# Kernel tuning notes

Hardware: AMD Instinct MI355X
Metric: run time of the kernel (lower is better)

## Reference

```python
import jax, jax.numpy as jnp
import numpy as np

N = 50000      # nodes
E = 800000     # edges (avg degree 16)
D = 128        # hidden_dim (= in_dim)
H = 8          # heads
DH = D // H    # head dim = 16
L = 2          # num_layers=1 -> ModuleList has 2 layers (extra append)
LN_EPS = 1e-5


def layer_norm(x, w, b):
    m = jnp.mean(x, axis=-1, keepdims=True)
    v = jnp.mean((x - m) ** 2, axis=-1, keepdims=True)
    return (x - m) * jax.lax.rsqrt(v + LN_EPS) * w + b


def setup_inputs() -> dict:
    key = jax.random.key(0)
    ks = jax.random.split(key, 16)
    s = 0.05

    def nrm(k, shape):
        return jax.random.normal(k, shape, jnp.float32) * s

    inp = {
        "h": jax.random.normal(ks[0], (N, D), jnp.float32),
        "src": jax.random.randint(ks[1], (E,), 0, N),
        "dst": jax.random.randint(ks[2], (E,), 0, N),
        "W_emb": nrm(ks[3], (D, D)),
        "Wq": nrm(ks[4], (L, D, D)), "bq": jnp.zeros((L, D), jnp.float32),
        "Wk": nrm(ks[5], (L, D, D)), "bk": jnp.zeros((L, D), jnp.float32),
        "Wv": nrm(ks[6], (L, D, D)), "bv": jnp.zeros((L, D), jnp.float32),
        "Wo": nrm(ks[7], (L, D, D)), "bo": jnp.zeros((L, D), jnp.float32),
        "ln1_w": jnp.ones((L, D), jnp.float32), "ln1_b": jnp.zeros((L, D), jnp.float32),
        "Wf1": nrm(ks[8], (L, D, 2 * D)), "bf1": jnp.zeros((L, 2 * D), jnp.float32),
        "Wf2": nrm(ks[9], (L, 2 * D, D)), "bf2": jnp.zeros((L, D), jnp.float32),
        "ln2_w": jnp.ones((L, D), jnp.float32), "ln2_b": jnp.zeros((L, D), jnp.float32),
    }
    return inp


def reference(h, src, dst, W_emb, Wq, bq, Wk, bk, Wv, bv, Wo, bo,
              ln1_w, ln1_b, Wf1, bf1, Wf2, bf2, ln2_w, ln2_b):
    n = h.shape[0]
    scale = 1.0 / np.sqrt(DH)  # np.sqrt(self.out_dim), out_dim = head dim = 16
    h = h @ W_emb  # embedding_h (no bias)
    for l in range(L):
        q = (h @ Wq[l] + bq[l]).reshape(n, H, DH)
        k = (h @ Wk[l] + bk[l]).reshape(n, H, DH)
        v = (h @ Wv[l] + bv[l]).reshape(n, H, DH)
        # per-edge score: K[src] . Q[dst], scaled, clamped, exponentiated
        s = jnp.einsum('ehd,ehd->eh', k[src], q[dst]) * scale  # [E,H]
        s = jnp.exp(jnp.clip(s, -5.0, 5.0))
        # scatter-sum weighted V and normalizer z into dst nodes
        wV = jax.ops.segment_sum(v[src] * s[:, :, None], dst, num_segments=n)  # [N,H,DH]
        z = jax.ops.segment_sum(s, dst, num_segments=n)                        # [N,H]
        attn = (wV / (z[:, :, None] + 1e-6)).reshape(n, D)
        hx = layer_norm(h + attn @ Wo[l] + bo[l], ln1_w[l], ln1_b[l])
        ffn = jax.nn.relu(hx @ Wf1[l] + bf1[l]) @ Wf2[l] + bf2[l]  # dropout inactive (eval)
        h = layer_norm(hx + ffn, ln2_w[l], ln2_b[l])
    return h
```

## Files before the change

kernel.cpp:

```cpp
#include <hip/hip_runtime.h>
#include <math.h>

static constexpr int N_NODES = 50000;
static constexpr int N_EDGES = 800000;
static constexpr int DMODEL  = 128;
static constexpr int MTILES  = N_NODES / 16;
static constexpr int CAPLOG  = 6;
static constexpr int ESPLIT  = 400384;

typedef __attribute__((ext_vector_type(8))) short short8;
typedef __attribute__((ext_vector_type(4))) float float4v;

__device__ __forceinline__ unsigned short f2bf(float f) {
    unsigned u = __builtin_bit_cast(unsigned, f);
    u += 0x7fffu + ((u >> 16) & 1u);
    return (unsigned short)(u >> 16);
}
__device__ __forceinline__ float bf2f(unsigned short b) {
    unsigned u = ((unsigned)b) << 16;
    return __builtin_bit_cast(float, u);
}

struct PrepSeg { const float* src; int K; int N; int dstOff; };
struct PrepArgs { PrepSeg seg[13]; };

__global__ void prep_kernel(PrepArgs pa, unsigned short* wf, int* counts)
{
    if (blockIdx.y == 13) {
        for (int i = blockIdx.x * 256 + threadIdx.x; i < N_NODES; i += 128 * 256)
            counts[i] = 0;
        return;
    }
    PrepSeg sg = pa.seg[blockIdx.y];
    int e = blockIdx.x * 256 + threadIdx.x;
    int total = sg.K * sg.N;
    if (e >= total) return;
    int n = e % sg.N;
    int k = e / sg.N;
    int ks = sg.K >> 5;
    int nt = n >> 4, c = n & 15, s = k >> 5, q = (k >> 3) & 3, jj = k & 7;
    int di = sg.dstOff + (nt * ks + s) * 512 + q * 128 + c * 8 + jj;
    wf[di] = f2bf(sg.src[e]);
}

__device__ __forceinline__ void scatter_body(
    const int* __restrict__ src, const int* __restrict__ dst,
    int* counts, int* eslot, int ebeg, int eend)
{
    int blk = ebeg + blockIdx.x * 1024;
    if (blk >= eend) return;
    int base = blk + threadIdx.x;
    int d[4], s[4];
    bool v[4];
#pragma unroll
    for (int k = 0; k < 4; ++k) {
        int e = base + k * 256;
        v[k] = e < eend;
        int ec = v[k] ? e : ebeg;
        d[k] = dst[ec];
        s[k] = src[ec];
    }
#pragma unroll
    for (int k = 0; k < 4; ++k) {
        if (v[k]) {
            int r = atomicAdd(&counts[d[k]], 1);
            eslot[(d[k] << CAPLOG) + r] = s[k];
        }
    }
}

template<int KSTEPS, int NT, int EPI, bool AF32, bool WRF, bool WRB>
__device__ __forceinline__ void gemm_body(
    const void* __restrict__ Ap, const unsigned short* __restrict__ Wfc,
    const float* __restrict__ bias, const float* res,
    float* Cf, unsigned short* Cb,
    const float* __restrict__ lnw, const float* __restrict__ lnb,
    int ldA, int ldC, int mtiles, int colBase)
{
    const int lane = threadIdx.x & 63;
    const int c = lane & 15;
    const int q = lane >> 4;

    __shared__ unsigned short smB[NT * KSTEPS * 512];
    {
        const int totalVec = NT * KSTEPS * 64;
        const uint4* gsrc = (const uint4*)Wfc;
        uint4* sdst = (uint4*)smB;
#pragma unroll
        for (int i = threadIdx.x; i < totalVec; i += 256)
            sdst[i] = gsrc[i];
    }
    __syncthreads();

    short8 bfrag[NT][KSTEPS];
#pragma unroll
    for (int nt = 0; nt < NT; ++nt)
#pragma unroll
        for (int s = 0; s < KSTEPS; ++s)
            bfrag[nt][s] = *(const short8*)(smB + (nt * KSTEPS + s) * 512 + lane * 8);

    float bb[NT];
#pragma unroll
    for (int nt = 0; nt < NT; ++nt)
        bb[nt] = bias ? bias[colBase + nt * 16 + c] : 0.f;

    float lw[NT], lb[NT];
    if (EPI == 3) {
#pragma unroll
        for (int nt = 0; nt < NT; ++nt) {
            lw[nt] = lnw[nt * 16 + c];
            lb[nt] = lnb[nt * 16 + c];
        }
    }

    const int wid = blockIdx.x * 4 + (threadIdx.x >> 6);
    const int nw  = gridDim.x * 4;

    for (int mt = wid; mt < mtiles; mt += nw) {
        const int row0 = mt * 16;
        short8 afrag[KSTEPS];
        if (AF32) {
            const float* A32 = (const float*)Ap;
#pragma unroll
            for (int s = 0; s < KSTEPS; ++s) {
                const float4* p = (const float4*)(A32 + (size_t)(row0 + c) * ldA + s * 32 + q * 8);
                float4 x0 = p[0], x1 = p[1];
                short8 a;
                a[0] = (short)f2bf(x0.x); a[1] = (short)f2bf(x0.y);
                a[2] = (short)f2bf(x0.z); a[3] = (short)f2bf(x0.w);
                a[4] = (short)f2bf(x1.x); a[5] = (short)f2bf(x1.y);
                a[6] = (short)f2bf(x1.z); a[7] = (short)f2bf(x1.w);
                afrag[s] = a;
            }
        } else {
            const unsigned short* Ab = (const unsigned short*)Ap;
#pragma unroll
            for (int s = 0; s < KSTEPS; ++s)
                afrag[s] = *(const short8*)(Ab + (size_t)(row0 + c) * ldA + s * 32 + q * 8);
        }

        float4v acc[NT];
#pragma unroll
        for (int nt = 0; nt < NT; ++nt) acc[nt] = (float4v)0.f;
#pragma unroll
        for (int s = 0; s < KSTEPS; ++s)
#pragma unroll
            for (int nt = 0; nt < NT; ++nt)
                acc[nt] = __builtin_amdgcn_mfma_f32_16x16x32_bf16(afrag[s], bfrag[nt][s], acc[nt], 0, 0, 0);

#pragma unroll
        for (int nt = 0; nt < NT; ++nt) {
            const int col = colBase + nt * 16 + c;
#pragma unroll
            for (int r = 0; r < 4; ++r) {
                const int grow = row0 + q * 4 + r;
                float v = acc[nt][r] + bb[nt];
                if (EPI == 2 || EPI == 3) v += res[(size_t)grow * ldC + col];
                if (EPI == 1) v = fmaxf(v, 0.f);
                acc[nt][r] = v;
            }
        }

        if (EPI == 3) {
#pragma unroll
            for (int r = 0; r < 4; ++r) {
                float s = 0.f, ss = 0.f;
#pragma unroll
                for (int nt = 0; nt < NT; ++nt) {
                    float v = acc[nt][r];
                    s += v; ss = fmaf(v, v, ss);
                }
#pragma unroll
                for (int o = 1; o < 16; o <<= 1) {
                    s  += __shfl_xor(s, o, 64);
                    ss += __shfl_xor(ss, o, 64);
                }
                float m   = s * (1.0f / 128.0f);
                float var = ss * (1.0f / 128.0f) - m * m;
                float rs  = rsqrtf(var + 1e-5f);
                const int grow = row0 + q * 4 + r;
#pragma unroll
                for (int nt = 0; nt < NT; ++nt) {
                    float v = (acc[nt][r] - m) * rs * lw[nt] + lb[nt];
                    if (WRF) Cf[(size_t)grow * ldC + nt * 16 + c] = v;
                    if (WRB) Cb[(size_t)grow * ldC + nt * 16 + c] = f2bf(v);
                }
            }
        } else {
#pragma unroll
            for (int nt = 0; nt < NT; ++nt) {
                const int col = colBase + nt * 16 + c;
#pragma unroll
                for (int r = 0; r < 4; ++r) {
                    const int grow = row0 + q * 4 + r;
                    if (WRF) Cf[(size_t)grow * ldC + col] = acc[nt][r];
                    if (WRB) Cb[(size_t)grow * ldC + col] = f2bf(acc[nt][r]);
                }
            }
        }
    }
}

__global__ __launch_bounds__(256, 2)
void emb_sc_gemm(const float* __restrict__ A, const unsigned short* __restrict__ Wf,
                 float* Cf, unsigned short* Cb, int mtiles,
                 const int* __restrict__ src, const int* __restrict__ dst,
                 int* counts, int* eslot, int ebeg, int eend)
{
    if (blockIdx.y == 1) {
        scatter_body(src, dst, counts, eslot, ebeg, eend);
        return;
    }
    gemm_body<4, 8, 0, true, true, true>(
        A, Wf, nullptr, nullptr, Cf, Cb, nullptr, nullptr, 128, 128, mtiles, 0);
}

struct QkvPtrs { const float* bias[3]; unsigned short* out[3]; int ldc[3]; };

__global__ __launch_bounds__(256, 2)
void qkv_sc_gemm(const unsigned short* __restrict__ A, const unsigned short* __restrict__ WfBase,
                 QkvPtrs ptrs, int mtiles,
                 const int* __restrict__ src, const int* __restrict__ dst,
                 int* counts, int* eslot, int ebeg, int eend)
{
    if (blockIdx.y == 3) {
        scatter_body(src, dst, counts, eslot, ebeg, eend);
        return;
    }
    const int sel = blockIdx.y;
    gemm_body<4, 8, 0, false, false, true>(
        A, WfBase + (size_t)sel * 32768, ptrs.bias[sel], nullptr,
        nullptr, ptrs.out[sel], nullptr, nullptr, 128, ptrs.ldc[sel], mtiles, 0);
}

template<bool WRB>
__global__ __launch_bounds__(256, 2)
void blk_kernel(const unsigned short* __restrict__ attn,
                const unsigned short* __restrict__ W0,
                const unsigned short* __restrict__ W1,
                const unsigned short* __restrict__ W2,
                const float* __restrict__ b0,
                const float* __restrict__ b1, const float* __restrict__ b2,
                const float* __restrict__ l1wv, const float* __restrict__ l1bv,
                const float* __restrict__ l2wv, const float* __restrict__ l2bv,
                const float* __restrict__ res,
                float* Cf, unsigned short* Cb,
                int mtiles)
{
    const int lane = threadIdx.x & 63;
    const int c = lane & 15;
    const int q = lane >> 4;
    const int w = threadIdx.x >> 6;

    __shared__ unsigned short hxf[4 * 64 * 8];
    __shared__ unsigned short exf[8 * 64 * 8];
    __shared__ float sred1[16][4][2];
    __shared__ float sred2[16][4][2];

    short8 b0f[2][4];
#pragma unroll
    for (int nt = 0; nt < 2; ++nt)
#pragma unroll
        for (int s = 0; s < 4; ++s)
            b0f[nt][s] = *(const short8*)(W0 + (size_t)((w * 2 + nt) * 4 + s) * 512 + lane * 8);

    short8 b1f[4][4];
#pragma unroll
    for (int nt = 0; nt < 4; ++nt)
#pragma unroll
        for (int s = 0; s < 4; ++s)
            b1f[nt][s] = *(const short8*)(W1 + (size_t)((w * 4 + nt) * 4 + s) * 512 + lane * 8);

    short8 b2f[2][8];
#pragma unroll
    for (int nt = 0; nt < 2; ++nt)
#pragma unroll
        for (int s = 0; s < 8; ++s)
            b2f[nt][s] = *(const short8*)(W2 + (size_t)((w * 2 + nt) * 8 + s) * 512 + lane * 8);

    float bb0[2], l1w[2], l1b[2], bb2[2], l2w[2], l2b[2];
#pragma unroll
    for (int nt = 0; nt < 2; ++nt) {
        int col = w * 32 + nt * 16 + c;
        bb0[nt] = b0[col];  l1w[nt] = l1wv[col]; l1b[nt] = l1bv[col];
        bb2[nt] = b2[col];  l2w[nt] = l2wv[col]; l2b[nt] = l2bv[col];
    }
    float bb1[4];
#pragma unroll
    for (int nt = 0; nt < 4; ++nt) bb1[nt] = b1[w * 64 + nt * 16 + c];

    const int iters = (mtiles + gridDim.x - 1) / gridDim.x;
    for (int it = 0; it < iters; ++it) {
        const int mt = blockIdx.x + it * gridDim.x;
        const bool active = mt < mtiles;
        const int row0 = (active ? mt : 0) * 16;

        short8 af0[4];
#pragma unroll
        for (int s = 0; s < 4; ++s)
            af0[s] = *(const short8*)(attn + (size_t)(row0 + c) * 128 + s * 32 + q * 8);

        float4v acc0[2];
#pragma unroll
        for (int nt = 0; nt < 2; ++nt) acc0[nt] = (float4v)0.f;
#pragma unroll
        for (int s = 0; s < 4; ++s)
#pragma unroll
            for (int nt = 0; nt < 2; ++nt)
                acc0[nt] = __builtin_amdgcn_mfma_f32_16x16x32_bf16(af0[s], b0f[nt][s], acc0[nt], 0, 0, 0);

        float vv0[2][4];
#pragma unroll
        for (int nt = 0; nt < 2; ++nt)
#pragma unroll
            for (int r = 0; r < 4; ++r)
                vv0[nt][r] = acc0[nt][r] + bb0[nt] +
                             res[(size_t)(row0 + q * 4 + r) * 128 + w * 32 + nt * 16 + c];

#pragma unroll
        for (int r = 0; r < 4; ++r) {
            float s  = vv0[0][r] + vv0[1][r];
            float ss = fmaf(vv0[0][r], vv0[0][r], vv0[1][r] * vv0[1][r]);
#pragma unroll
            for (int o = 1; o < 16; o <<= 1) {
                s  += __shfl_xor(s, o, 64);
                ss += __shfl_xor(ss, o, 64);
            }
            if (c == 0) {
                sred1[q * 4 + r][w][0] = s;
                sred1[q * 4 + r][w][1] = ss;
            }
        }
        __syncthreads();

        float hx[2][4];
#pragma unroll
        for (int r = 0; r < 4; ++r) {
            const int rr = q * 4 + r;
            float S  = sred1[rr][0][0] + sred1[rr][1][0] + sred1[rr][2][0] + sred1[rr][3][0];
            float SS = sred1[rr][0][1] + sred1[rr][1][1] + sred1[rr][2][1] + sred1[rr][3][1];
            float m   = S * (1.0f / 128.0f);
            float var = SS * (1.0f / 128.0f) - m * m;
            float rs  = rsqrtf(var + 1e-5f);
#pragma unroll
            for (int nt = 0; nt < 2; ++nt)
                hx[nt][r] = (vv0[nt][r] - m) * rs * l1w[nt] + l1b[nt];
        }
#pragma unroll
        for (int nt = 0; nt < 2; ++nt) {
            const int col = w * 32 + nt * 16 + c;
            const int base = ((col >> 5) * 4 + ((col >> 3) & 3)) * 16;
            const int j = col & 7;
#pragma unroll
            for (int r = 0; r < 4; ++r)
                hxf[(size_t)(base + q * 4 + r) * 8 + j] = f2bf(hx[nt][r]);
        }
        __syncthreads();

        short8 af1[4];
#pragma unroll
        for (int s = 0; s < 4; ++s)
            af1[s] = *(const short8*)(hxf + (size_t)(s * 64 + lane) * 8);

        float4v acc1[4];
#pragma unroll
        for (int nt = 0; nt < 4; ++nt) acc1[nt] = (float4v)0.f;
#pragma unroll
        for (int s = 0; s < 4; ++s)
#pragma unroll
            for (int nt = 0; nt < 4; ++nt)
                acc1[nt] = __builtin_amdgcn_mfma_f32_16x16x32_bf16(af1[s], b1f[nt][s], acc1[nt], 0, 0, 0);

#pragma unroll
        for (int nt = 0; nt < 4; ++nt) {
            const int col = w * 64 + nt * 16 + c;
            const int base = ((col >> 5) * 4 + ((col >> 3) & 3)) * 16;
            const int j = col & 7;
#pragma unroll
            for (int r = 0; r < 4; ++r) {
                float v = fmaxf(acc1[nt][r] + bb1[nt], 0.f);
                exf[(size_t)(base + q * 4 + r) * 8 + j] = f2bf(v);
            }
        }
        __syncthreads();

        short8 af2[8];
#pragma unroll
        for (int s = 0; s < 8; ++s)
            af2[s] = *(const short8*)(exf + (size_t)(s * 64 + lane) * 8);

        float4v acc2[2];
#pragma unroll
        for (int nt = 0; nt < 2; ++nt) acc2[nt] = (float4v)0.f;
#pragma unroll
        for (int s = 0; s < 8; ++s)
#pragma unroll
            for (int nt = 0; nt < 2; ++nt)
                acc2[nt] = __builtin_amdgcn_mfma_f32_16x16x32_bf16(af2[s], b2f[nt][s], acc2[nt], 0, 0, 0);

        float vv2[2][4];
#pragma unroll
        for (int nt = 0; nt < 2; ++nt)
#pragma unroll
            for (int r = 0; r < 4; ++r)
                vv2[nt][r] = acc2[nt][r] + bb2[nt] + hx[nt][r];

#pragma unroll
        for (int r = 0; r < 4; ++r) {
            float s  = vv2[0][r] + vv2[1][r];
            float ss = fmaf(vv2[0][r], vv2[0][r], vv2[1][r] * vv2[1][r]);
#pragma unroll
            for (int o = 1; o < 16; o <<= 1) {
                s  += __shfl_xor(s, o, 64);
                ss += __shfl_xor(ss, o, 64);
            }
            if (c == 0) {
                sred2[q * 4 + r][w][0] = s;
                sred2[q * 4 + r][w][1] = ss;
            }
        }
        __syncthreads();

#pragma unroll
        for (int r = 0; r < 4; ++r) {
            const int rr = q * 4 + r;
            float S  = sred2[rr][0][0] + sred2[rr][1][0] + sred2[rr][2][0] + sred2[rr][3][0];
            float SS = sred2[rr][0][1] + sred2[rr][1][1] + sred2[rr][2][1] + sred2[rr][3][1];
            float m   = S * (1.0f / 128.0f);
            float var = SS * (1.0f / 128.0f) - m * m;
            float rs  = rsqrtf(var + 1e-5f);
            if (active) {
                const int grow = row0 + rr;
#pragma unroll
                for (int nt = 0; nt < 2; ++nt) {
                    const int col = w * 32 + nt * 16 + c;
                    float v = (vv2[nt][r] - m) * rs * l2w[nt] + l2b[nt];
                    Cf[(size_t)grow * 128 + col] = v;
                    if (WRB) Cb[(size_t)grow * 128 + col] = f2bf(v);
                }
            }
        }
    }
}

__global__ __launch_bounds__(256)
void agg_kernel(const unsigned short* qv, const unsigned short* __restrict__ kvv,
                const int* __restrict__ counts, const int* __restrict__ eslot,
                unsigned short* attn, int n_nodes)
{
    int w    = (int)((blockIdx.x * 256 + threadIdx.x) >> 6);
    int lane = threadIdx.x & 63;
    if (w >= n_nodes) return;
    const int g  = lane >> 4;
    const int li = lane & 15;

    float qf[8];
    {
        uint4 qb = *(const uint4*)(qv + (size_t)w * 128 + li * 8);
        const unsigned* qp = (const unsigned*)&qb;
#pragma unroll
        for (int j = 0; j < 4; ++j) {
            qf[2 * j]     = bf2f((unsigned short)(qp[j] & 0xffff));
            qf[2 * j + 1] = bf2f((unsigned short)(qp[j] >> 16));
        }
    }

    const int beg = w << CAPLOG;
    const int end = beg + counts[w];
    float acc[8] = {0.f, 0.f, 0.f, 0.f, 0.f, 0.f, 0.f, 0.f};
    float z = 0.f;

    for (int e = beg; e < end; e += 8) {
        int  i0 = e + g;
        int  i1 = e + g + 4;
        bool v0 = i0 < end;
        bool v1 = i1 < end;
        int  s0 = eslot[v0 ? i0 : beg];
        int  s1 = eslot[v1 ? i1 : beg];

        const unsigned short* b0 = kvv + (size_t)s0 * 256 + li * 8;
        const unsigned short* b1 = kvv + (size_t)s1 * 256 + li * 8;
        uint4 kb0 = *(const uint4*)(b0);
        uint4 vb0 = *(const uint4*)(b0 + 128);
        uint4 kb1 = *(const uint4*)(b1);
        uint4 vb1 = *(const uint4*)(b1 + 128);

        const unsigned* kp0 = (const unsigned*)&kb0;
        const unsigned* kp1 = (const unsigned*)&kb1;
        float p0 = 0.f, p1 = 0.f;
#pragma unroll
        for (int j = 0; j < 4; ++j) {
            p0 = fmaf(bf2f((unsigned short)(kp0[j] & 0xffff)), qf[2 * j],     p0);
            p0 = fmaf(bf2f((unsigned short)(kp0[j] >> 16)),    qf[2 * j + 1], p0);
            p1 = fmaf(bf2f((unsigned short)(kp1[j] & 0xffff)), qf[2 * j],     p1);
            p1 = fmaf(bf2f((unsigned short)(kp1[j] >> 16)),    qf[2 * j + 1], p1);
        }
        p0 += __shfl_xor(p0, 1, 64);
        p1 += __shfl_xor(p1, 1, 64);

        float sv0 = __expf(fminf(fmaxf(p0 * 0.25f, -5.f), 5.f));
        float sv1 = __expf(fminf(fmaxf(p1 * 0.25f, -5.f), 5.f));
        sv0 = v0 ? sv0 : 0.f;
        sv1 = v1 ? sv1 : 0.f;

        const unsigned* vp0 = (const unsigned*)&vb0;
        const unsigned* vp1 = (const unsigned*)&vb1;
#pragma unroll
        for (int j = 0; j < 4; ++j) {
            acc[2 * j]     = fmaf(sv0, bf2f((unsigned short)(vp0[j] & 0xffff)), acc[2 * j]);
            acc[2 * j + 1] = fmaf(sv0, bf2f((unsigned short)(vp0[j] >> 16)),    acc[2 * j + 1]);
            acc[2 * j]     = fmaf(sv1, bf2f((unsigned short)(vp1[j] & 0xffff)), acc[2 * j]);
            acc[2 * j + 1] = fmaf(sv1, bf2f((unsigned short)(vp1[j] >> 16)),    acc[2 * j + 1]);
        }
        z += sv0 + sv1;
    }

#pragma unroll
    for (int o = 16; o < 64; o <<= 1) {
#pragma unroll
        for (int j = 0; j < 8; ++j) acc[j] += __shfl_xor(acc[j], o, 64);
        z += __shfl_xor(z, o, 64);
    }

    if (g == 0) {
        float inv = 1.f / (z + 1e-6f);
        unsigned ow[4];
#pragma unroll
        for (int j = 0; j < 4; ++j)
            ow[j] = (unsigned)f2bf(acc[2 * j] * inv) |
                    ((unsigned)f2bf(acc[2 * j + 1] * inv) << 16);
        *(uint4*)(attn + (size_t)w * 128 + li * 8) = *(const uint4*)ow;
    }
}

extern "C" void kernel_launch(void* const* d_in, const int* in_sizes, int n_in,
                              void* d_out, int out_size, void* d_ws, size_t ws_size,
                              hipStream_t stream)
{
    const float* h_in  = (const float*)d_in[0];
    const int*   src   = (const int*)d_in[1];
    const int*   dst   = (const int*)d_in[2];
    const float* W_emb = (const float*)d_in[3];
    const float* Wq    = (const float*)d_in[4];
    const float* bq    = (const float*)d_in[5];
    const float* Wk    = (const float*)d_in[6];
    const float* bk    = (const float*)d_in[7];
    const float* Wv    = (const float*)d_in[8];
    const float* bv    = (const float*)d_in[9];
    const float* Wo    = (const float*)d_in[10];
    const float* bo    = (const float*)d_in[11];
    const float* ln1w  = (const float*)d_in[12];
    const float* ln1b  = (const float*)d_in[13];
    const float* Wf1   = (const float*)d_in[14];
    const float* bf1   = (const float*)d_in[15];
    const float* Wf2   = (const float*)d_in[16];
    const float* bf2   = (const float*)d_in[17];
    const float* ln2w  = (const float*)d_in[18];
    const float* ln2b  = (const float*)d_in[19];
    float* out = (float*)d_out;

    const int N = N_NODES, E = N_EDGES;
    const size_t NF = (size_t)N * DMODEL;

    float*          hbuf  = (float*)d_ws;
    unsigned short* hbf   = (unsigned short*)(hbuf + NF);
    unsigned short* qbuf  = hbf + NF;
    unsigned short* kvbuf = qbuf + NF;
    unsigned short* wf    = kvbuf + 2 * NF;
    int* counts = (int*)(wf + 278528);
    int* eslot  = (int*)d_out;

    const int EMB_O = 0, Q_O = 16384, K_O = 49152, V_O = 81920, O_O = 114688,
              F1_O = 147456, F2_O = 212992;

    const int GX = 391;

    PrepArgs pa;
    pa.seg[0]  = {W_emb,          128, 128, EMB_O};
    pa.seg[1]  = {Wq,             128, 128, Q_O};
    pa.seg[2]  = {Wq + 16384,     128, 128, Q_O + 16384};
    pa.seg[3]  = {Wk,             128, 128, K_O};
    pa.seg[4]  = {Wk + 16384,     128, 128, K_O + 16384};
    pa.seg[5]  = {Wv,             128, 128, V_O};
    pa.seg[6]  = {Wv + 16384,     128, 128, V_O + 16384};
    pa.seg[7]  = {Wo,             128, 128, O_O};
    pa.seg[8]  = {Wo + 16384,     128, 128, O_O + 16384};
    pa.seg[9]  = {Wf1,            128, 256, F1_O};
    pa.seg[10] = {Wf1 + 32768,    128, 256, F1_O + 32768};
    pa.seg[11] = {Wf2,            256, 128, F2_O};
    pa.seg[12] = {Wf2 + 32768,    256, 128, F2_O + 32768};
    prep_kernel<<<dim3(128, 14), 256, 0, stream>>>(pa, wf, counts);

    emb_sc_gemm<<<dim3(GX, 2), 256, 0, stream>>>(
        h_in, wf + EMB_O, hbuf, hbf, MTILES, src, dst, counts, eslot, 0, ESPLIT);

    const int rowBlocks = (N + 3) / 4;
    for (int l = 0; l < 2; ++l) {
        QkvPtrs qp;
        qp.bias[0] = bq + l * 128; qp.bias[1] = bk + l * 128; qp.bias[2] = bv + l * 128;
        qp.out[0] = qbuf;   qp.ldc[0] = 128;
        qp.out[1] = kvbuf;  qp.ldc[1] = 256;
        qp.out[2] = kvbuf + 128; qp.ldc[2] = 256;
        qkv_sc_gemm<<<dim3(GX, l == 0 ? 4 : 3), 256, 0, stream>>>(
            hbf, wf + Q_O + l * 16384, qp, MTILES, src, dst, counts, eslot,
            l == 0 ? ESPLIT : 0, l == 0 ? E : 0);

        agg_kernel<<<rowBlocks, 256, 0, stream>>>(qbuf, kvbuf, counts, eslot, qbuf, N);

        if (l == 0)
            blk_kernel<true><<<dim3(GX, 1), 256, 0, stream>>>(
                qbuf, wf + O_O, wf + F1_O, wf + F2_O,
                bo, bf1, bf2, ln1w, ln1b, ln2w, ln2b,
                hbuf, hbuf, hbf, MTILES);
        else
            blk_kernel<false><<<dim3(GX, 1), 256, 0, stream>>>(
                qbuf, wf + O_O + 16384, wf + F1_O + 32768, wf + F2_O + 32768,
                bo + 128, bf1 + 256, bf2 + 128, ln1w + 128, ln1b + 128,
                ln2w + 128, ln2b + 128, hbuf, out, nullptr, MTILES);
    }
}
```

Before: 385.1 us.

## Fuse embedding GEMM with layer-0 QKV projection in one kernel

```diff
diff --git a/kernel.cpp b/kernel.cpp
--- a/kernel.cpp
+++ b/kernel.cpp
@@ -104,15 +104,6 @@
     for (int nt = 0; nt < NT; ++nt)
         bb[nt] = bias ? bias[colBase + nt * 16 + c] : 0.f;
 
-    float lw[NT], lb[NT];
-    if (EPI == 3) {
-#pragma unroll
-        for (int nt = 0; nt < NT; ++nt) {
-            lw[nt] = lnw[nt * 16 + c];
-            lb[nt] = lnb[nt * 16 + c];
-        }
-    }
-
     const int wid = blockIdx.x * 4 + (threadIdx.x >> 6);
     const int nw  = gridDim.x * 4;
 
@@ -155,82 +146,158 @@
             for (int r = 0; r < 4; ++r) {
                 const int grow = row0 + q * 4 + r;
                 float v = acc[nt][r] + bb[nt];
-                if (EPI == 2 || EPI == 3) v += res[(size_t)grow * ldC + col];
                 if (EPI == 1) v = fmaxf(v, 0.f);
-                acc[nt][r] = v;
-            }
-        }
-
-        if (EPI == 3) {
-#pragma unroll
-            for (int r = 0; r < 4; ++r) {
-                float s = 0.f, ss = 0.f;
-#pragma unroll
-                for (int nt = 0; nt < NT; ++nt) {
-                    float v = acc[nt][r];
-                    s += v; ss = fmaf(v, v, ss);
-                }
-#pragma unroll
-                for (int o = 1; o < 16; o <<= 1) {
-                    s  += __shfl_xor(s, o, 64);
-                    ss += __shfl_xor(ss, o, 64);
-                }
-                float m   = s * (1.0f / 128.0f);
-                float var = ss * (1.0f / 128.0f) - m * m;
-                float rs  = rsqrtf(var + 1e-5f);
-                const int grow = row0 + q * 4 + r;
-#pragma unroll
-                for (int nt = 0; nt < NT; ++nt) {
-                    float v = (acc[nt][r] - m) * rs * lw[nt] + lb[nt];
-                    if (WRF) Cf[(size_t)grow * ldC + nt * 16 + c] = v;
-                    if (WRB) Cb[(size_t)grow * ldC + nt * 16 + c] = f2bf(v);
-                }
-            }
-        } else {
-#pragma unroll
-            for (int nt = 0; nt < NT; ++nt) {
-                const int col = colBase + nt * 16 + c;
-#pragma unroll
-                for (int r = 0; r < 4; ++r) {
-                    const int grow = row0 + q * 4 + r;
-                    if (WRF) Cf[(size_t)grow * ldC + col] = acc[nt][r];
-                    if (WRB) Cb[(size_t)grow * ldC + col] = f2bf(acc[nt][r]);
-                }
-            }
-        }
-    }
-}
+                if (WRF) Cf[(size_t)grow * ldC + col] = v;
+                if (WRB) Cb[(size_t)grow * ldC + col] = f2bf(v);
+            }
+        }
+    }
+}
+
+struct QkvPtrs { const float* bias[3]; unsigned short* out[3]; int ldc[3]; };
 
 __global__ __launch_bounds__(256, 2)
-void emb_sc_gemm(const float* __restrict__ A, const unsigned short* __restrict__ Wf,
-                 float* Cf, unsigned short* Cb, int mtiles,
-                 const int* __restrict__ src, const int* __restrict__ dst,
-                 int* counts, int* eslot, int ebeg, int eend)
-{
-    if (blockIdx.y == 1) {
-        scatter_body(src, dst, counts, eslot, ebeg, eend);
-        return;
-    }
-    gemm_body<4, 8, 0, true, true, true>(
-        A, Wf, nullptr, nullptr, Cf, Cb, nullptr, nullptr, 128, 128, mtiles, 0);
-}
-
-struct QkvPtrs { const float* bias[3]; unsigned short* out[3]; int ldc[3]; };
-
-__global__ __launch_bounds__(256, 2)
-void qkv_sc_gemm(const unsigned short* __restrict__ A, const unsigned short* __restrict__ WfBase,
-                 QkvPtrs ptrs, int mtiles,
-                 const int* __restrict__ src, const int* __restrict__ dst,
-                 int* counts, int* eslot, int ebeg, int eend)
-{
-    if (blockIdx.y == 3) {
-        scatter_body(src, dst, counts, eslot, ebeg, eend);
-        return;
-    }
+void qkv_gemm(const unsigned short* __restrict__ A, const unsigned short* __restrict__ WfBase,
+              QkvPtrs ptrs, int mtiles)
+{
     const int sel = blockIdx.y;
     gemm_body<4, 8, 0, false, false, true>(
         A, WfBase + (size_t)sel * 32768, ptrs.bias[sel], nullptr,
         nullptr, ptrs.out[sel], nullptr, nullptr, 128, ptrs.ldc[sel], mtiles, 0);
+}
+
+__global__ __launch_bounds__(256, 2)
+void embqkv_kernel(const float* __restrict__ hin,
+                   const unsigned short* __restrict__ We,
+                   const unsigned short* __restrict__ Wq_,
+                   const unsigned short* __restrict__ Wk_,
+                   const unsigned short* __restrict__ Wv_,
+                   const float* __restrict__ bqv, const float* __restrict__ bkv,
+                   const float* __restrict__ bvv,
+                   float* houtf, unsigned short* houtb,
+                   unsigned short* qout, unsigned short* kvout,
+                   const int* __restrict__ esrc, const int* __restrict__ edst,
+                   int* counts, int* eslot, int mtiles)
+{
+    if (blockIdx.y == 1) { scatter_body(esrc, edst, counts, eslot, 0, ESPLIT); return; }
+    if (blockIdx.y == 2) { scatter_body(esrc, edst, counts, eslot, ESPLIT, N_EDGES); return; }
+
+    const int lane = threadIdx.x & 63;
+    const int c = lane & 15;
+    const int q = lane >> 4;
+    const int w = threadIdx.x >> 6;
+
+    __shared__ unsigned short hf[4 * 64 * 8];
+
+    short8 bef[2][4];
+#pragma unroll
+    for (int nt = 0; nt < 2; ++nt)
+#pragma unroll
+        for (int s = 0; s < 4; ++s)
+            bef[nt][s] = *(const short8*)(We + (size_t)((w * 2 + nt) * 4 + s) * 512 + lane * 8);
+
+    short8 bqk[6][4];
+#pragma unroll
+    for (int m = 0; m < 3; ++m) {
+        const unsigned short* Wm = (m == 0) ? Wq_ : (m == 1) ? Wk_ : Wv_;
+#pragma unroll
+        for (int nt = 0; nt < 2; ++nt)
+#pragma unroll
+            for (int s = 0; s < 4; ++s)
+                bqk[m * 2 + nt][s] = *(const short8*)(Wm + (size_t)((w * 2 + nt) * 4 + s) * 512 + lane * 8);
+    }
+
+    float bqk_b[6];
+#pragma unroll
+    for (int nt = 0; nt < 2; ++nt) {
+        int col = w * 32 + nt * 16 + c;
+        bqk_b[0 + nt] = bqv[col];
+        bqk_b[2 + nt] = bkv[col];
+        bqk_b[4 + nt] = bvv[col];
+    }
+
+    const int iters = (mtiles + gridDim.x - 1) / gridDim.x;
+    for (int it = 0; it < iters; ++it) {
+        const int mt = blockIdx.x + it * gridDim.x;
+        const bool active = mt < mtiles;
+        const int row0 = (active ? mt : 0) * 16;
+
+        short8 af[4];
+        {
+            const float* A32 = hin;
+#pragma unroll
+            for (int s = 0; s < 4; ++s) {
+                const float4* p = (const float4*)(A32 + (size_t)(row0 + c) * 128 + s * 32 + q * 8);
+                float4 x0 = p[0], x1 = p[1];
+                short8 a;
+                a[0] = (short)f2bf(x0.x); a[1] = (short)f2bf(x0.y);
+                a[2] = (short)f2bf(x0.z); a[3] = (short)f2bf(x0.w);
+                a[4] = (short)f2bf(x1.x); a[5] = (short)f2bf(x1.y);
+                a[6] = (short)f2bf(x1.z); a[7] = (short)f2bf(x1.w);
+                af[s] = a;
+            }
+        }
+
+        float4v acc0[2];
+#pragma unroll
+        for (int nt = 0; nt < 2; ++nt) acc0[nt] = (float4v)0.f;
+#pragma unroll
+        for (int s = 0; s < 4; ++s)
+#pragma unroll
+            for (int nt = 0; nt < 2; ++nt)
+                acc0[nt] = __builtin_amdgcn_mfma_f32_16x16x32_bf16(af[s], bef[nt][s], acc0[nt], 0, 0, 0);
+
+#pragma unroll
+        for (int nt = 0; nt < 2; ++nt) {
+            const int col = w * 32 + nt * 16 + c;
+            const int base = ((col >> 5) * 4 + ((col >> 3) & 3)) * 16;
+            const int j = col & 7;
+#pragma unroll
+            for (int r = 0; r < 4; ++r) {
+                float v = acc0[nt][r];
+                unsigned short vb = f2bf(v);
+                hf[(size_t)(base + q * 4 + r) * 8 + j] = vb;
+                if (active) {
+                    const int grow = row0 + q * 4 + r;
+                    houtf[(size_t)grow * 128 + col] = v;
+                    houtb[(size_t)grow * 128 + col] = vb;
+                }
+            }
+        }
+        __syncthreads();
+
+        short8 aq[4];
+#pragma unroll
+        for (int s = 0; s < 4; ++s)
+            aq[s] = *(const short8*)(hf + (size_t)(s * 64 + lane) * 8);
+
+        float4v acc1[6];
+#pragma unroll
+        for (int x = 0; x < 6; ++x) acc1[x] = (float4v)0.f;
+#pragma unroll
+        for (int s = 0; s < 4; ++s)
+#pragma unroll
+            for (int x = 0; x < 6; ++x)
+                acc1[x] = __builtin_amdgcn_mfma_f32_16x16x32_bf16(aq[s], bqk[x][s], acc1[x], 0, 0, 0);
+
+        if (active) {
+#pragma unroll
+            for (int m = 0; m < 3; ++m)
+#pragma unroll
+                for (int nt = 0; nt < 2; ++nt) {
+                    const int col = w * 32 + nt * 16 + c;
+#pragma unroll
+                    for (int r = 0; r < 4; ++r) {
+                        const int grow = row0 + q * 4 + r;
+                        float v = acc1[m * 2 + nt][r] + bqk_b[m * 2 + nt];
+                        if (m == 0)      qout[(size_t)grow * 128 + col]        = f2bf(v);
+                        else if (m == 1) kvout[(size_t)grow * 256 + col]       = f2bf(v);
+                        else             kvout[(size_t)grow * 256 + 128 + col] = f2bf(v);
+                    }
+                }
+        }
+        __syncthreads();
+    }
 }
 
 template<bool WRB>
@@ -591,19 +658,22 @@
     pa.seg[12] = {Wf2 + 32768,    256, 128, F2_O + 32768};
     prep_kernel<<<dim3(128, 14), 256, 0, stream>>>(pa, wf, counts);
 
-    emb_sc_gemm<<<dim3(GX, 2), 256, 0, stream>>>(
-        h_in, wf + EMB_O, hbuf, hbf, MTILES, src, dst, counts, eslot, 0, ESPLIT);
+    embqkv_kernel<<<dim3(GX, 3), 256, 0, stream>>>(
+        h_in, wf + EMB_O, wf + Q_O, wf + K_O, wf + V_O,
+        bq, bk, bv, hbuf, hbf, qbuf, kvbuf,
+        src, dst, counts, eslot, MTILES);
 
     const int rowBlocks = (N + 3) / 4;
     for (int l = 0; l < 2; ++l) {
-        QkvPtrs qp;
-        qp.bias[0] = bq + l * 128; qp.bias[1] = bk + l * 128; qp.bias[2] = bv + l * 128;
-        qp.out[0] = qbuf;   qp.ldc[0] = 128;
-        qp.out[1] = kvbuf;  qp.ldc[1] = 256;
-        qp.out[2] = kvbuf + 128; qp.ldc[2] = 256;
-        qkv_sc_gemm<<<dim3(GX, l == 0 ? 4 : 3), 256, 0, stream>>>(
-            hbf, wf + Q_O + l * 16384, qp, MTILES, src, dst, counts, eslot,
-            l == 0 ? ESPLIT : 0, l == 0 ? E : 0);
+        if (l == 1) {
+            QkvPtrs qp;
+            qp.bias[0] = bq + 128; qp.bias[1] = bk + 128; qp.bias[2] = bv + 128;
+            qp.out[0] = qbuf;   qp.ldc[0] = 128;
+            qp.out[1] = kvbuf;  qp.ldc[1] = 256;
+            qp.out[2] = kvbuf + 128; qp.ldc[2] = 256;
+            qkv_gemm<<<dim3(GX, 3), 256, 0, stream>>>(
+                hbf, wf + Q_O + 16384, qp, MTILES);
+        }
 
         agg_kernel<<<rowBlocks, 256, 0, stream>>>(qbuf, kvbuf, counts, eslot, qbuf, N);
 
```

Result: faster. 367.6 us (-4.6%).
